# Optimization experiments

Hardware: AMD Instinct MI355X
Metric: run time of the kernel (lower is better)

The kernel has to match this reference:

```python
import jax, jax.numpy as jnp
import numpy as np

B, N, D_PTS, D_MODEL, K = 2, 8192, 3, 128, 16


def _gather(points, idx):
    # points: (B, N, C), idx: (B, M, K) -> (B, M, K, C)
    return jax.vmap(lambda p, i: p[i])(points, idx)


def setup_inputs() -> dict:
    key = jax.random.key(0)
    ks = jax.random.split(key, 20)

    def w(k, shape, fan_in):
        bound = 1.0 / np.sqrt(fan_in)
        return jax.random.uniform(k, shape, jnp.float32, -bound, bound)

    return {
        "xyz": jax.random.normal(ks[0], (B, D_PTS, N), jnp.float32),
        "features": jax.random.normal(ks[1], (B, D_PTS, N), jnp.float32),
        "fc1_w": w(ks[2], (D_MODEL, D_PTS), D_PTS),
        "fc1_b": w(ks[3], (D_MODEL,), D_PTS),
        "fc2_w": w(ks[4], (D_PTS, D_MODEL), D_MODEL),
        "fc2_b": w(ks[5], (D_PTS,), D_MODEL),
        "d1_w": w(ks[6], (D_MODEL, 3), 3),
        "d1_b": w(ks[7], (D_MODEL,), 3),
        "d2_w": w(ks[8], (D_MODEL, D_MODEL), D_MODEL),
        "d2_b": w(ks[9], (D_MODEL,), D_MODEL),
        "g1_w": w(ks[10], (D_MODEL, D_MODEL), D_MODEL),
        "g1_b": w(ks[11], (D_MODEL,), D_MODEL),
        "g2_w": w(ks[12], (D_MODEL, D_MODEL), D_MODEL),
        "g2_b": w(ks[13], (D_MODEL,), D_MODEL),
        "wq_w": w(ks[14], (D_MODEL, D_MODEL), D_MODEL),
        "wk_w": w(ks[15], (D_MODEL, D_MODEL), D_MODEL),
        "wv_w": w(ks[16], (D_MODEL, D_MODEL), D_MODEL),
    }


def reference(xyz, features, fc1_w, fc1_b, fc2_w, fc2_b,
              d1_w, d1_b, d2_w, d2_b, g1_w, g1_b, g2_w, g2_b,
              wq_w, wk_w, wv_w):
    xyz_p = jnp.swapaxes(xyz, 1, 2)        # (B, N, 3)
    feat = jnp.swapaxes(features, 1, 2)    # (B, N, d_points)

    # square_distance(xyz, xyz): ||a||^2 + ||b||^2 - 2 a.b
    sq = jnp.sum(xyz_p * xyz_p, axis=-1)   # (B, N)
    dists = sq[:, :, None] + sq[:, None, :] - 2.0 * jnp.einsum('bnc,bmc->bnm', xyz_p, xyz_p)
    _, knn_idx = jax.lax.top_k(-dists, K)  # (B, N, K) indices of k smallest dists

    knn_xyz = _gather(xyz_p, knn_idx)      # (B, N, K, 3)
    pre = feat

    x = feat @ fc1_w.T + fc1_b             # (B, N, d_model)
    q = x @ wq_w.T                         # (B, N, d_model)
    kg = _gather(x @ wk_w.T, knn_idx)      # (B, N, K, d_model)
    vg = _gather(x @ wv_w.T, knn_idx)      # (B, N, K, d_model)

    rel = xyz_p[:, :, None] - knn_xyz      # (B, N, K, 3)
    pos = jax.nn.relu(rel @ d1_w.T + d1_b) @ d2_w.T + d2_b          # fc_delta

    h = q[:, :, None] - kg + pos
    attn = jax.nn.relu(h @ g1_w.T + g1_b) @ g2_w.T + g2_b           # fc_gamma
    attn = jax.nn.softmax(attn / np.sqrt(D_MODEL), axis=-2)         # softmax over K

    res = jnp.einsum('bmnf,bmnf->bmf', attn, vg + pos)              # (B, N, d_model)
    res = res @ fc2_w.T + fc2_b + pre                               # (B, N, d_points)
    return jnp.swapaxes(res, 1, 2)                                  # (B, d_points, N)
```

## Files before the change

### kernel.cpp

```cpp
#include <hip/hip_runtime.h>
#include <cfloat>

#define NPTS 8192

typedef __attribute__((ext_vector_type(8))) short short8;
typedef __attribute__((ext_vector_type(4))) short short4v;
typedef __attribute__((ext_vector_type(4))) float f32x4;

__device__ inline unsigned short f2bf(float f) {
    unsigned u = __builtin_bit_cast(unsigned, f);
    u += 0x7fffu + ((u >> 16) & 1u);
    return (unsigned short)(u >> 16);
}
__device__ inline float bf2f(unsigned short h) {
    unsigned u = ((unsigned)h) << 16;
    return __builtin_bit_cast(float, u);
}

__global__ void prep_kernel(const float* __restrict__ d2_w,
                            const float* __restrict__ g1_w,
                            const float* __restrict__ g2_w,
                            unsigned short* __restrict__ wd2,
                            unsigned short* __restrict__ wg1,
                            unsigned short* __restrict__ wg2,
                            const float* __restrict__ xyz,
                            float4* __restrict__ candp,
                            const float* __restrict__ wq_w,
                            const float* __restrict__ wk_w,
                            const float* __restrict__ wv_w,
                            float* __restrict__ wqT,
                            float* __restrict__ wkT,
                            float* __restrict__ wvT)
{
    int i = blockIdx.x * 256 + threadIdx.x;
    if (i < 49152) {
        int sel = i >> 14, off = i & 16383;
        const float* s = (sel == 0) ? d2_w : (sel == 1) ? g1_w : g2_w;
        unsigned short* d = (sel == 0) ? wd2 : (sel == 1) ? wg1 : wg2;
        d[off] = f2bf(s[off]);
    } else if (i < 65536) {
        int j = i - 49152;
        int b = j >> 13, n = j & 8191;
        const float* xg = xyz + (long)b * 3 * NPTS;
        float x = xg[n], y = xg[NPTS + n], z = xg[2*NPTS + n];
        float4 c; c.x = x; c.y = y; c.z = z;
        c.w = fmaf(x, x, fmaf(y, y, z * z));
        candp[j] = c;
    } else if (i < 114688) {
        int idx = i - 65536;
        int sel = idx >> 14, off = idx & 16383;
        int k = off >> 7, c = off & 127;
        const float* s = (sel == 0) ? wq_w : (sel == 1) ? wk_w : wv_w;
        float* d = (sel == 0) ? wqT : (sel == 1) ? wkT : wvT;
        d[off] = s[c * 128 + k];
    }
}

#define KNB 120
#define KBBASE 952
#define KCAP 64

__global__ __launch_bounds__(512, 2)
void knn_proj_kernel(const float4* __restrict__ cand,
                     float* __restrict__ part_d, int* __restrict__ part_i,
                     const float* __restrict__ feat,
                     const float* __restrict__ fc1_w, const float* __restrict__ fc1_b,
                     const float* __restrict__ wqT, const float* __restrict__ wkT,
                     const float* __restrict__ wvT,
                     unsigned short* __restrict__ qb,
                     unsigned short* __restrict__ kbuf,
                     unsigned short* __restrict__ vbuf)
{
    __shared__ union {
        struct {
            unsigned hist[KNB * 64];
            float2   surv[64 * 65];
            unsigned scnt[64];
            int      bthr[64];
        } k;
        struct {
            float fl[32][3];
            float xl[32][128];
        } p;
    } sm;

    const int t = threadIdx.x;

    if (blockIdx.x < 512) {
        unsigned* hist = sm.k.hist;
        float2*   surv = sm.k.surv;
        unsigned* scnt = sm.k.scnt;
        int*      bthr = sm.k.bthr;

        const int ql = t & 63, wv = t >> 6;
        const int wv_u = __builtin_amdgcn_readfirstlane(wv);
        const int qsg = blockIdx.x >> 1;
        const int ck  = blockIdx.x & 1;
        const int b_u = qsg >> 7;
        const int q   = qsg * 64 + ql;
        const int n   = q & 8191;

        const float4* cp = cand + (b_u << 13) + ck * 4096 + wv_u * 512;
        const int ibase = ck * 4096 + wv_u * 512;
        float4 qc = cand[(b_u << 13) + n];
        const float qx2 = -2.f * qc.x, qy2 = -2.f * qc.y, qz2 = -2.f * qc.z;
        const float qw = qc.w;

        for (int i = t; i < KNB * 64; i += 512) hist[i] = 0u;
        if (t < 64) scnt[t] = 0u;
        __syncthreads();

        auto dtil = [&](float4 c) {
            return fmaf(qx2, c.x, fmaf(qy2, c.y, fmaf(qz2, c.z, c.w + qw)));
        };
        auto binOf = [&](float d) {
            float dc = fmaxf(d, 1e-30f);
            int b = (int)(__builtin_bit_cast(unsigned, dc) >> 20) - KBBASE;
            return b < 0 ? 0 : (b > (KNB - 1) ? (KNB - 1) : b);
        };

        {
            unsigned* hq = hist + ql;
            float4 A[8], Bv[8];
            #pragma unroll
            for (int u = 0; u < 8; ++u) A[u] = cp[u];
            for (int m = 0; m < 512; m += 16) {
                #pragma unroll
                for (int u = 0; u < 8; ++u) Bv[u] = cp[m + 8 + u];
                #pragma unroll
                for (int u = 0; u < 8; ++u) {
                    int bb = binOf(dtil(A[u]));
                    atomicAdd(hq + bb * 64, 1u);
                }
                if (m + 16 < 512) {
                    #pragma unroll
                    for (int u = 0; u < 8; ++u) A[u] = cp[m + 16 + u];
                }
                #pragma unroll
                for (int u = 0; u < 8; ++u) {
                    int bb = binOf(dtil(Bv[u]));
                    atomicAdd(hq + bb * 64, 1u);
                }
            }
        }
        __syncthreads();

        if (t < 64) {
            int cum = 0, bs = 0;
            #pragma unroll 8
            for (int b = 0; b < KNB; ++b) {
                cum += (int)hist[b * 64 + t];
                bs += (cum < 16) ? 1 : 0;
            }
            bthr[t] = (bs >= KNB - 1) ? 0x7FFFFFFF : ((bs + KBBASE + 1) << 20);
        }
        __syncthreads();

        {
            const int mythr = bthr[ql];
            float4 A[8], Bv[8];
            #pragma unroll
            for (int u = 0; u < 8; ++u) A[u] = cp[u];
            for (int m = 0; m < 512; m += 16) {
                #pragma unroll
                for (int u = 0; u < 8; ++u) Bv[u] = cp[m + 8 + u];
                #pragma unroll
                for (int u = 0; u < 8; ++u) {
                    float d = dtil(A[u]);
                    if (__builtin_bit_cast(int, d) < mythr) {
                        unsigned s = atomicAdd(&scnt[ql], 1u);
                        if (s < (unsigned)KCAP) {
                            float2 e; e.x = d;
                            e.y = __builtin_bit_cast(float, ibase + m + u);
                            surv[ql * 65 + s] = e;
                        }
                    }
                }
                if (m + 16 < 512) {
                    #pragma unroll
                    for (int u = 0; u < 8; ++u) A[u] = cp[m + 16 + u];
                }
                #pragma unroll
                for (int u = 0; u < 8; ++u) {
                    float d = dtil(Bv[u]);
                    if (__builtin_bit_cast(int, d) < mythr) {
                        unsigned s = atomicAdd(&scnt[ql], 1u);
                        if (s < (unsigned)KCAP) {
                            float2 e; e.x = d;
                            e.y = __builtin_bit_cast(float, ibase + m + 8 + u);
                            surv[ql * 65 + s] = e;
                        }
                    }
                }
            }
        }
        __syncthreads();

        {
            const int q2 = t >> 3;
            const int s0 = t & 7;
            const unsigned cnt = min(scnt[q2], (unsigned)KCAP);
            const float2* sp = surv + q2 * 65;
            const long pb = ((long)(qsg * 64 + q2)) * 32 + ck * 16;
            for (unsigned s = s0; s < cnt; s += 8) {
                float2 e = sp[s];
                float d = e.x;
                int idx = __builtin_bit_cast(int, e.y);
                int rank = 0;
                #pragma unroll 8
                for (unsigned j = 0; j < cnt; ++j) {
                    float2 f = sp[j];
                    float dj = f.x;
                    int ij = __builtin_bit_cast(int, f.y);
                    rank += ((dj < d) || (dj == d && ij < idx)) ? 1 : 0;
                }
                if (rank < 16) {
                    part_d[pb + rank] = d;
                    part_i[pb + rank] = idx;
                }
            }
        }
    } else {
        float (*fl)[3]   = sm.p.fl;
        float (*xl)[128] = sm.p.xl;

        const int tc = t & 127;
        const int pg = t >> 7;
        const long base = (long)(blockIdx.x - 512) * 32 + pg * 8;

        if (tc < 24) {
            int p = tc / 3, d = tc % 3;
            long pt = base + p;
            int b = (int)(pt >> 13), n = (int)(pt & 8191);
            fl[pg*8 + p][d] = feat[((long)b * 3 + d) * NPTS + n];
        }
        __syncthreads();

        float w0 = fc1_w[tc*3+0], w1 = fc1_w[tc*3+1], w2 = fc1_w[tc*3+2];
        float b0 = fc1_b[tc];
        #pragma unroll
        for (int p = 0; p < 8; ++p)
            xl[pg*8 + p][tc] = fmaf(w0, fl[pg*8+p][0],
                               fmaf(w1, fl[pg*8+p][1],
                               fmaf(w2, fl[pg*8+p][2], b0)));
        __syncthreads();

        float aq[8], ak[8], av[8];
        #pragma unroll
        for (int p = 0; p < 8; ++p) { aq[p] = 0.f; ak[p] = 0.f; av[p] = 0.f; }

        for (int i4 = 0; i4 < 32; ++i4) {
            const int k0 = i4 * 4;
            float qa = wqT[(k0+0)*128 + tc], qbw = wqT[(k0+1)*128 + tc];
            float qc2 = wqT[(k0+2)*128 + tc], qd = wqT[(k0+3)*128 + tc];
            float ka = wkT[(k0+0)*128 + tc], kbw = wkT[(k0+1)*128 + tc];
            float kc2 = wkT[(k0+2)*128 + tc], kd = wkT[(k0+3)*128 + tc];
            float va = wvT[(k0+0)*128 + tc], vbw = wvT[(k0+1)*128 + tc];
            float vc2 = wvT[(k0+2)*128 + tc], vd = wvT[(k0+3)*128 + tc];
            #pragma unroll
            for (int p = 0; p < 8; ++p) {
                float4 x = *(const float4*)&xl[pg*8 + p][k0];
                aq[p] = fmaf(qa,x.x, fmaf(qbw,x.y, fmaf(qc2,x.z, fmaf(qd,x.w, aq[p]))));
                ak[p] = fmaf(ka,x.x, fmaf(kbw,x.y, fmaf(kc2,x.z, fmaf(kd,x.w, ak[p]))));
                av[p] = fmaf(va,x.x, fmaf(vbw,x.y, fmaf(vc2,x.z, fmaf(vd,x.w, av[p]))));
            }
        }
        const int perm = (tc & 15) * 8 + (tc >> 4);
        #pragma unroll
        for (int p = 0; p < 8; ++p) {
            long pt = base + p;
            qb[pt*128 + perm]   = f2bf(aq[p]);
            kbuf[pt*128 + perm] = f2bf(ak[p]);
            vbuf[pt*128 + perm] = f2bf(av[p]);
        }
    }
}

__global__ __launch_bounds__(256, 4)
void knn_merge_kernel(const float* __restrict__ part_d,
                      const int* __restrict__ part_i, int* __restrict__ knn)
{
    __shared__ float sd[8][33];
    __shared__ int   si[8][33];
    const int t = threadIdx.x;
    const int qq = t >> 5, e = t & 31;
    const long q = (long)blockIdx.x * 8 + qq;
    float d = part_d[q * 32 + e];
    int idx = part_i[q * 32 + e];
    sd[qq][e] = d; si[qq][e] = idx;
    __syncthreads();
    int rank = 0;
    #pragma unroll
    for (int j = 0; j < 32; ++j) {
        float dj = sd[qq][j];
        rank += ((dj < d) || (dj == d && si[qq][j] < idx)) ? 1 : 0;
    }
    if (rank < 16) knn[q * 16 + rank] = idx;
}

__device__ inline int hswz(int r, int c) {
    return r * 128 + (c ^ ((r & 7) << 4));
}
__device__ inline int wswz(int r, int c) {
    return r * 128 + (c ^ ((r & 7) << 3));
}

__global__ __launch_bounds__(256, 2)
void attn_kernel(const float* __restrict__ xyz, const float* __restrict__ feat,
                 const float* __restrict__ d1_w, const float* __restrict__ d1_b,
                 const float* __restrict__ d2_b, const float* __restrict__ g1_b,
                 const float* __restrict__ g2_b,
                 const float* __restrict__ fc2_w, const float* __restrict__ fc2_b,
                 const unsigned short* __restrict__ qb,
                 const unsigned short* __restrict__ kb,
                 const unsigned short* __restrict__ vb,
                 const unsigned short* __restrict__ wd2,
                 const unsigned short* __restrict__ wg1,
                 const unsigned short* __restrict__ wg2,
                 const int* __restrict__ knn, float* __restrict__ out)
{
    __shared__ unsigned short hbuf_all[4][32 * 128];
    __shared__ unsigned short wbuf[128 * 128];

    const int wave = threadIdx.x >> 6;
    const int lane = threadIdx.x & 63;
    unsigned short* hbuf = hbuf_all[wave];

    const int quad = lane >> 4, l15 = lane & 15;
    const long pbase = (long)blockIdx.x * 8 + wave * 2;
    const int b = (int)(pbase >> 13);
    const long bofs = (long)b * NPTS;

    auto stageW = [&](const unsigned short* w) {
        #pragma unroll
        for (int it = 0; it < 8; ++it) {
            int cidx = (int)threadIdx.x + it * 256;
            int row = cidx >> 4, c8 = (cidx & 15) << 3;
            short8 v = *(const short8*)(w + cidx * 8);
            *(short8*)&wbuf[wswz(row, c8)] = v;
        }
    };

    int m = 0; float rx = 0.f, ry = 0.f, rz = 0.f;
    if (lane < 32) {
        m = knn[(pbase + (lane >> 4)) * 16 + (lane & 15)];
        int nn = (int)((pbase + (lane >> 4)) & 8191);
        const float* xg = xyz + (long)b * 3 * NPTS;
        rx = xg[nn]        - xg[m];
        ry = xg[NPTS+nn]   - xg[NPTS+m];
        rz = xg[2*NPTS+nn] - xg[2*NPTS+m];
    }

    int koff[8];
    #pragma unroll
    for (int mt = 0; mt < 2; ++mt)
        #pragma unroll
        for (int r = 0; r < 4; ++r) {
            int idxm = __shfl(m, mt*16 + quad*4 + r);
            koff[mt*4 + r] = (int)(bofs + idxm) * 128 + l15*8;
        }

    short8 qvv[2], kgv[2][4], vgv[2][4];
    #pragma unroll
    for (int mt = 0; mt < 2; ++mt) {
        qvv[mt] = *(const short8*)(qb + (size_t)(pbase + mt) * 128 + l15*8);
        #pragma unroll
        for (int r = 0; r < 4; ++r)
            kgv[mt][r] = *(const short8*)(kb + koff[mt*4 + r]);
    }

    stageW(wd2);

    {
        float w0[8], w1[8], w2[8], bb[8];
        #pragma unroll
        for (int k = 0; k < 8; ++k) {
            int c = l15*8 + k;
            w0[k] = d1_w[c*3]; w1[k] = d1_w[c*3+1]; w2[k] = d1_w[c*3+2];
            bb[k] = d1_b[c];
        }
        #pragma unroll
        for (int i = 0; i < 8; ++i) {
            int row = quad + 4*i;
            float sx = __shfl(rx, row), sy = __shfl(ry, row), sz = __shfl(rz, row);
            short8 hv;
            #pragma unroll
            for (int k = 0; k < 8; ++k) {
                float v = fmaf(w0[k], sx, fmaf(w1[k], sy, fmaf(w2[k], sz, bb[k])));
                hv[k] = (short)f2bf(fmaxf(v, 0.f));
            }
            *(short8*)&hbuf[hswz(row, l15*8)] = hv;
        }
    }
    __syncthreads();

    short8 A[2][4];
    f32x4 acc[2];

    auto loadA = [&]() {
        #pragma unroll
        for (int mt = 0; mt < 2; ++mt)
            #pragma unroll
            for (int kk = 0; kk < 4; ++kk)
                A[mt][kk] = *(const short8*)&hbuf[hswz(mt*16 + l15, kk*32 + quad*8)];
    };
    auto loadB = [&](int n0, short8& B0, short8& B1, short8& B2, short8& B3) {
        int r = n0*16 + l15;
        B0 = *(const short8*)&wbuf[wswz(r, quad*8)];
        B1 = *(const short8*)&wbuf[wswz(r, quad*8 + 32)];
        B2 = *(const short8*)&wbuf[wswz(r, quad*8 + 64)];
        B3 = *(const short8*)&wbuf[wswz(r, quad*8 + 96)];
    };

    unsigned posp[2][8][2];

    loadA();
    #pragma unroll
    for (int n0 = 0; n0 < 8; ++n0) {
        short8 B0, B1, B2, B3;
        loadB(n0, B0, B1, B2, B3);
        acc[0] = (f32x4){0.f,0.f,0.f,0.f};
        acc[1] = (f32x4){0.f,0.f,0.f,0.f};
        __builtin_amdgcn_s_setprio(1);
        #pragma unroll
        for (int mt = 0; mt < 2; ++mt) {
            acc[mt] = __builtin_amdgcn_mfma_f32_16x16x32_bf16(A[mt][0], B0, acc[mt], 0, 0, 0);
            acc[mt] = __builtin_amdgcn_mfma_f32_16x16x32_bf16(A[mt][1], B1, acc[mt], 0, 0, 0);
            acc[mt] = __builtin_amdgcn_mfma_f32_16x16x32_bf16(A[mt][2], B2, acc[mt], 0, 0, 0);
            acc[mt] = __builtin_amdgcn_mfma_f32_16x16x32_bf16(A[mt][3], B3, acc[mt], 0, 0, 0);
        }
        __builtin_amdgcn_s_setprio(0);
        int c = n0*16 + l15;
        float bb = d2_b[c];
        #pragma unroll
        for (int mt = 0; mt < 2; ++mt) {
            float qv = bf2f((unsigned short)qvv[mt][n0]);
            float p0 = acc[mt][0] + bb, p1 = acc[mt][1] + bb;
            float p2 = acc[mt][2] + bb, p3 = acc[mt][3] + bb;
            posp[mt][n0][0] = (unsigned)f2bf(p0) | ((unsigned)f2bf(p1) << 16);
            posp[mt][n0][1] = (unsigned)f2bf(p2) | ((unsigned)f2bf(p3) << 16);
            int rb = mt*16 + quad*4;
            hbuf[hswz(rb+0, c)] = f2bf(qv - bf2f((unsigned short)kgv[mt][0][n0]) + p0);
            hbuf[hswz(rb+1, c)] = f2bf(qv - bf2f((unsigned short)kgv[mt][1][n0]) + p1);
            hbuf[hswz(rb+2, c)] = f2bf(qv - bf2f((unsigned short)kgv[mt][2][n0]) + p2);
            hbuf[hswz(rb+3, c)] = f2bf(qv - bf2f((unsigned short)kgv[mt][3][n0]) + p3);
        }
    }
    __syncthreads();
    stageW(wg1);
    __syncthreads();

    loadA();
    #pragma unroll
    for (int n0 = 0; n0 < 8; ++n0) {
        short8 B0, B1, B2, B3;
        loadB(n0, B0, B1, B2, B3);
        acc[0] = (f32x4){0.f,0.f,0.f,0.f};
        acc[1] = (f32x4){0.f,0.f,0.f,0.f};
        __builtin_amdgcn_s_setprio(1);
        #pragma unroll
        for (int mt = 0; mt < 2; ++mt) {
            acc[mt] = __builtin_amdgcn_mfma_f32_16x16x32_bf16(A[mt][0], B0, acc[mt], 0, 0, 0);
            acc[mt] = __builtin_amdgcn_mfma_f32_16x16x32_bf16(A[mt][1], B1, acc[mt], 0, 0, 0);
            acc[mt] = __builtin_amdgcn_mfma_f32_16x16x32_bf16(A[mt][2], B2, acc[mt], 0, 0, 0);
            acc[mt] = __builtin_amdgcn_mfma_f32_16x16x32_bf16(A[mt][3], B3, acc[mt], 0, 0, 0);
        }
        __builtin_amdgcn_s_setprio(0);
        int c = n0*16 + l15;
        float bb = g1_b[c];
        #pragma unroll
        for (int mt = 0; mt < 2; ++mt) {
            int rb = mt*16 + quad*4;
            #pragma unroll
            for (int r = 0; r < 4; ++r)
                hbuf[hswz(rb+r, c)] = f2bf(fmaxf(acc[mt][r] + bb, 0.f));
        }
    }
    __syncthreads();
    stageW(wg2);

    #pragma unroll
    for (int mt = 0; mt < 2; ++mt)
        #pragma unroll
        for (int r = 0; r < 4; ++r)
            vgv[mt][r] = *(const short8*)(vb + koff[mt*4 + r]);
    __syncthreads();

    loadA();
    const float sc = 0.08838834764831845f;
    float pr[2][3];
    #pragma unroll
    for (int mt = 0; mt < 2; ++mt) { pr[mt][0] = 0.f; pr[mt][1] = 0.f; pr[mt][2] = 0.f; }
    #pragma unroll
    for (int n0 = 0; n0 < 8; ++n0) {
        short8 B0, B1, B2, B3;
        loadB(n0, B0, B1, B2, B3);
        acc[0] = (f32x4){0.f,0.f,0.f,0.f};
        acc[1] = (f32x4){0.f,0.f,0.f,0.f};
        __builtin_amdgcn_s_setprio(1);
        #pragma unroll
        for (int mt = 0; mt < 2; ++mt) {
            acc[mt] = __builtin_amdgcn_mfma_f32_16x16x32_bf16(A[mt][0], B0, acc[mt], 0, 0, 0);
            acc[mt] = __builtin_amdgcn_mfma_f32_16x16x32_bf16(A[mt][1], B1, acc[mt], 0, 0, 0);
            acc[mt] = __builtin_amdgcn_mfma_f32_16x16x32_bf16(A[mt][2], B2, acc[mt], 0, 0, 0);
            acc[mt] = __builtin_amdgcn_mfma_f32_16x16x32_bf16(A[mt][3], B3, acc[mt], 0, 0, 0);
        }
        __builtin_amdgcn_s_setprio(0);
        int c = n0*16 + l15;
        float bb = g2_b[c];
        float f0 = fc2_w[c];
        float f1 = fc2_w[128 + c];
        float f2 = fc2_w[256 + c];
        #pragma unroll
        for (int mt = 0; mt < 2; ++mt) {
            float e0 = (acc[mt][0] + bb) * sc;
            float e1 = (acc[mt][1] + bb) * sc;
            float e2 = (acc[mt][2] + bb) * sc;
            float e3 = (acc[mt][3] + bb) * sc;
            float mx = fmaxf(fmaxf(e0, e1), fmaxf(e2, e3));
            mx = fmaxf(mx, __shfl_xor(mx, 16));
            mx = fmaxf(mx, __shfl_xor(mx, 32));
            e0 = __expf(e0 - mx); e1 = __expf(e1 - mx);
            e2 = __expf(e2 - mx); e3 = __expf(e3 - mx);
            float ssum = e0 + e1 + e2 + e3;
            ssum += __shfl_xor(ssum, 16);
            ssum += __shfl_xor(ssum, 32);
            float p0 = bf2f((unsigned short)(posp[mt][n0][0] & 0xffff));
            float p1 = bf2f((unsigned short)(posp[mt][n0][0] >> 16));
            float p2 = bf2f((unsigned short)(posp[mt][n0][1] & 0xffff));
            float p3 = bf2f((unsigned short)(posp[mt][n0][1] >> 16));
            float p = e0 * (bf2f((unsigned short)vgv[mt][0][n0]) + p0)
                    + e1 * (bf2f((unsigned short)vgv[mt][1][n0]) + p1)
                    + e2 * (bf2f((unsigned short)vgv[mt][2][n0]) + p2)
                    + e3 * (bf2f((unsigned short)vgv[mt][3][n0]) + p3);
            p += __shfl_xor(p, 16);
            p += __shfl_xor(p, 32);
            float rres = p / ssum;
            pr[mt][0] = fmaf(f0, rres, pr[mt][0]);
            pr[mt][1] = fmaf(f1, rres, pr[mt][1]);
            pr[mt][2] = fmaf(f2, rres, pr[mt][2]);
        }
    }

    #pragma unroll
    for (int mt = 0; mt < 2; ++mt) {
        float pr0 = pr[mt][0], pr1 = pr[mt][1], pr2 = pr[mt][2];
        #pragma unroll
        for (int s2 = 1; s2 <= 8; s2 <<= 1) {
            pr0 += __shfl_xor(pr0, s2);
            pr1 += __shfl_xor(pr1, s2);
            pr2 += __shfl_xor(pr2, s2);
        }
        int nn = (int)((pbase + mt) & 8191);
        if (lane < 3) {
            float pv = (lane == 0) ? pr0 : (lane == 1) ? pr1 : pr2;
            long o = ((long)b*3 + lane) * NPTS + nn;
            out[o] = pv + fc2_b[lane] + feat[o];
        }
    }
}

extern "C" void kernel_launch(void* const* d_in, const int* in_sizes, int n_in,
                              void* d_out, int out_size, void* d_ws, size_t ws_size,
                              hipStream_t stream)
{
    const float* xyz   = (const float*)d_in[0];
    const float* feat  = (const float*)d_in[1];
    const float* fc1_w = (const float*)d_in[2];
    const float* fc1_b = (const float*)d_in[3];
    const float* fc2_w = (const float*)d_in[4];
    const float* fc2_b = (const float*)d_in[5];
    const float* d1_w  = (const float*)d_in[6];
    const float* d1_b  = (const float*)d_in[7];
    const float* d2_w  = (const float*)d_in[8];
    const float* d2_b  = (const float*)d_in[9];
    const float* g1_w  = (const float*)d_in[10];
    const float* g1_b  = (const float*)d_in[11];
    const float* g2_w  = (const float*)d_in[12];
    const float* g2_b  = (const float*)d_in[13];
    const float* wq_w  = (const float*)d_in[14];
    const float* wk_w  = (const float*)d_in[15];
    const float* wv_w  = (const float*)d_in[16];
    float* out = (float*)d_out;

    unsigned short* qb  = (unsigned short*)d_ws;
    unsigned short* kb  = qb + (size_t)16384*128;
    unsigned short* vb  = kb + (size_t)16384*128;
    unsigned short* wd2 = vb + (size_t)16384*128;
    unsigned short* wg1 = wd2 + 16384;
    unsigned short* wg2 = wg1 + 16384;
    int*   knn_ws = (int*)(wg2 + 16384);
    float4* cand  = (float4*)(knn_ws + (size_t)16384*16);
    float* part_d = (float*)(cand + 16384);
    int*   part_i = (int*)(part_d + (size_t)16384*64);
    float* wqT    = part_d + (size_t)16384*32;
    float* wkT    = wqT + 16384;
    float* wvT    = wkT + 16384;

    hipLaunchKernelGGL(prep_kernel, dim3(448), dim3(256), 0, stream,
                       d2_w, g1_w, g2_w, wd2, wg1, wg2, xyz, cand,
                       wq_w, wk_w, wv_w, wqT, wkT, wvT);
    hipLaunchKernelGGL(knn_proj_kernel, dim3(1024), dim3(512), 0, stream,
                       cand, part_d, part_i,
                       feat, fc1_w, fc1_b, wqT, wkT, wvT, qb, kb, vb);
    hipLaunchKernelGGL(knn_merge_kernel, dim3(2048), dim3(256), 0, stream,
                       part_d, part_i, knn_ws);
    hipLaunchKernelGGL(attn_kernel, dim3(2048), dim3(256), 0, stream,
                       xyz, feat, d1_w, d1_b, d2_b, g1_b, g2_b, fc2_w, fc2_b,
                       qb, kb, vb, wd2, wg1, wg2, knn_ws, out);
}
```

Before: 262.0 us.

## Fuse KNN partial merge into knn_proj via last-block atomic counter

Removes the separate knn_merge kernel launch. A per-query-group counter, zeroed in prep_kernel, tells whichever of the two candidate-half blocks finishes second to merge the 32 partial candidates into the final top-16 in shared memory. The bin computation also drops the fmaxf clamp and uses a signed bit shift, so negative distances fall into bin 0. The fusion saves a launch and a global round-trip, at the cost of threadfences, extra syncs and a serial tail in the last block.

```diff
diff --git a/kernel.cpp b/kernel.cpp
--- a/kernel.cpp
+++ b/kernel.cpp
@@ -30,7 +30,8 @@
                             const float* __restrict__ wv_w,
                             float* __restrict__ wqT,
                             float* __restrict__ wkT,
-                            float* __restrict__ wvT)
+                            float* __restrict__ wvT,
+                            unsigned* __restrict__ qcnt)
 {
     int i = blockIdx.x * 256 + threadIdx.x;
     if (i < 49152) {
@@ -53,6 +54,8 @@
         const float* s = (sel == 0) ? wq_w : (sel == 1) ? wk_w : wv_w;
         float* d = (sel == 0) ? wqT : (sel == 1) ? wkT : wvT;
         d[off] = s[c * 128 + k];
+    } else if (i < 114944) {
+        qcnt[i - 114688] = 0u;
     }
 }
 
@@ -63,6 +66,7 @@
 __global__ __launch_bounds__(512, 2)
 void knn_proj_kernel(const float4* __restrict__ cand,
                      float* __restrict__ part_d, int* __restrict__ part_i,
+                     unsigned* __restrict__ qcnt, int* __restrict__ knn,
                      const float* __restrict__ feat,
                      const float* __restrict__ fc1_w, const float* __restrict__ fc1_b,
                      const float* __restrict__ wqT, const float* __restrict__ wkT,
@@ -83,6 +87,7 @@
             float xl[32][128];
         } p;
     } sm;
+    __shared__ unsigned lastFlag;
 
     const int t = threadIdx.x;
 
@@ -114,8 +119,8 @@
             return fmaf(qx2, c.x, fmaf(qy2, c.y, fmaf(qz2, c.z, c.w + qw)));
         };
         auto binOf = [&](float d) {
-            float dc = fmaxf(d, 1e-30f);
-            int b = (int)(__builtin_bit_cast(unsigned, dc) >> 20) - KBBASE;
+            int sb = __builtin_bit_cast(int, d);
+            int b = (sb >> 20) - KBBASE;
             return b < 0 ? 0 : (b > (KNB - 1) ? (KNB - 1) : b);
         };
 
@@ -220,6 +225,38 @@
                 }
             }
         }
+
+        __syncthreads();
+        __threadfence();
+        __syncthreads();
+        if (t == 0) lastFlag = atomicAdd(&qcnt[qsg], 1u);
+        __syncthreads();
+        if (lastFlag == 1u) {
+            __threadfence();
+            float* msd = reinterpret_cast<float*>(sm.k.surv);
+            int*   msi = reinterpret_cast<int*>(sm.k.surv + 1100);
+            for (int eg = t; eg < 2048; eg += 512) {
+                int q2 = eg >> 5, sl = eg & 31;
+                long gp = ((long)(qsg * 64 + q2)) * 32 + sl;
+                msd[q2 * 33 + sl] = part_d[gp];
+                msi[q2 * 33 + sl] = part_i[gp];
+            }
+            __syncthreads();
+            const int q2 = t >> 3, s0 = t & 7;
+            #pragma unroll
+            for (int j4 = 0; j4 < 4; ++j4) {
+                int sl = s0 + j4 * 8;
+                float d = msd[q2 * 33 + sl];
+                int idx = msi[q2 * 33 + sl];
+                int rank = 0;
+                #pragma unroll
+                for (int j = 0; j < 32; ++j) {
+                    float dj = msd[q2 * 33 + j];
+                    rank += ((dj < d) || (dj == d && msi[q2 * 33 + j] < idx)) ? 1 : 0;
+                }
+                if (rank < 16) knn[(long)(qsg * 64 + q2) * 16 + rank] = idx;
+            }
+        }
     } else {
         float (*fl)[3]   = sm.p.fl;
         float (*xl)[128] = sm.p.xl;
@@ -274,28 +311,6 @@
             vbuf[pt*128 + perm] = f2bf(av[p]);
         }
     }
-}
-
-__global__ __launch_bounds__(256, 4)
-void knn_merge_kernel(const float* __restrict__ part_d,
-                      const int* __restrict__ part_i, int* __restrict__ knn)
-{
-    __shared__ float sd[8][33];
-    __shared__ int   si[8][33];
-    const int t = threadIdx.x;
-    const int qq = t >> 5, e = t & 31;
-    const long q = (long)blockIdx.x * 8 + qq;
-    float d = part_d[q * 32 + e];
-    int idx = part_i[q * 32 + e];
-    sd[qq][e] = d; si[qq][e] = idx;
-    __syncthreads();
-    int rank = 0;
-    #pragma unroll
-    for (int j = 0; j < 32; ++j) {
-        float dj = sd[qq][j];
-        rank += ((dj < d) || (dj == d && si[qq][j] < idx)) ? 1 : 0;
-    }
-    if (rank < 16) knn[q * 16 + rank] = idx;
 }
 
 __device__ inline int hswz(int r, int c) {
@@ -596,15 +611,14 @@
     float* wqT    = part_d + (size_t)16384*32;
     float* wkT    = wqT + 16384;
     float* wvT    = wkT + 16384;
-
-    hipLaunchKernelGGL(prep_kernel, dim3(448), dim3(256), 0, stream,
+    unsigned* qcnt = (unsigned*)(part_i + (size_t)16384*32);
+
+    hipLaunchKernelGGL(prep_kernel, dim3(449), dim3(256), 0, stream,
                        d2_w, g1_w, g2_w, wd2, wg1, wg2, xyz, cand,
-                       wq_w, wk_w, wv_w, wqT, wkT, wvT);
+                       wq_w, wk_w, wv_w, wqT, wkT, wvT, qcnt);
     hipLaunchKernelGGL(knn_proj_kernel, dim3(1024), dim3(512), 0, stream,
-                       cand, part_d, part_i,
+                       cand, part_d, part_i, qcnt, knn_ws,
                        feat, fc1_w, fc1_b, wqT, wkT, wvT, qb, kb, vb);
-    hipLaunchKernelGGL(knn_merge_kernel, dim3(2048), dim3(256), 0, stream,
-                       part_d, part_i, knn_ws);
     hipLaunchKernelGGL(attn_kernel, dim3(2048), dim3(256), 0, stream,
                        xyz, feat, d1_w, d1_b, d2_b, g1_b, g2_b, fc2_w, fc2_b,
                        qb, kb, vb, wd2, wg1, wg2, knn_ws, out);
```

New measurement: 389.9 us. 48.8% more time.
